# Kernel tuning notes

Hardware: AMD Instinct MI355X
Metric: run time of the kernel (lower is better)

The kernel has to match this reference:

```python
import jax, jax.numpy as jnp
import numpy as np

D_MODEL, N_HEAD, D_HEAD = 192, 16, 6
INNER = N_HEAD * D_HEAD  # 96
LN_EPS = 1e-9
INF = 1e6


def _rel_pos_embeds(S):
    # Funnel get_position_embeds, relative_shift path, block 0
    half = D_MODEL // 2
    freq = jnp.arange(half, dtype=jnp.float32)
    inv_freq = 1.0 / (10000.0 ** (freq / half))
    rel_pos_id = jnp.arange(-2 * S, 2 * S, dtype=jnp.float32)  # [4S]
    sinusoid = rel_pos_id[:, None] * inv_freq[None, :]          # [4S, half]
    pos_embed = jnp.concatenate([jnp.sin(sinusoid), jnp.cos(sinusoid)], axis=-1)  # [4S, D]
    # block 0: relative_pos(pos, stride=1) = arange(S, -S, -1), offset by 2S
    idx = jnp.arange(S, -S, -1) + 2 * S  # [2S]
    return pos_embed[idx]  # [2S, D]


def _relative_shift_gather(pos_attn, context_len):
    # shift = 1 (q_len == context_len)
    B, n, S, M = pos_attn.shape  # M = 2*S
    pa = pos_attn.reshape(B, n, M, S)[:, :, 1:, :]
    pa = pa.reshape(B, n, S, M - 1)[..., :context_len]
    return pa


def setup_inputs() -> dict:
    key = jax.random.key(0)
    ks = jax.random.split(key, 12)
    B, S = 4, 1024
    s = 0.02
    return {
        "x": jax.random.normal(ks[0], (B, S, D_MODEL), dtype=jnp.float32),
        "mask0": jnp.ones((B, S), dtype=jnp.float32),
        "Wq": jax.random.normal(ks[1], (D_MODEL, INNER), dtype=jnp.float32) * s,
        "Wk": jax.random.normal(ks[2], (D_MODEL, INNER), dtype=jnp.float32) * s,
        "bk": jnp.zeros((INNER,), dtype=jnp.float32),
        "Wv": jax.random.normal(ks[3], (D_MODEL, INNER), dtype=jnp.float32) * s,
        "bv": jnp.zeros((INNER,), dtype=jnp.float32),
        "Wo": jax.random.normal(ks[4], (INNER, D_MODEL), dtype=jnp.float32) * s,
        "bo": jnp.zeros((D_MODEL,), dtype=jnp.float32),
        "r_w_bias": jax.random.normal(ks[5], (N_HEAD, D_HEAD), dtype=jnp.float32) * s,
        "r_r_bias": jax.random.normal(ks[6], (N_HEAD, D_HEAD), dtype=jnp.float32) * s,
        "r_kernel": jax.random.normal(ks[7], (D_MODEL, N_HEAD, D_HEAD), dtype=jnp.float32) * s,
        "gamma": jnp.ones((D_MODEL,), dtype=jnp.float32),
        "beta": jnp.zeros((D_MODEL,), dtype=jnp.float32),
    }


def reference(x, mask0, Wq, Wk, bk, Wv, bv, Wo, bo, r_w_bias, r_r_bias, r_kernel, gamma, beta):
    B, S, _ = x.shape
    scale = 1.0 / np.sqrt(D_HEAD).astype(np.float32)

    q = (x @ Wq).reshape(B, S, N_HEAD, D_HEAD) * scale       # q_head pre-scaled
    k = (x @ Wk + bk).reshape(B, S, N_HEAD, D_HEAD)
    v = (x @ Wv + bv).reshape(B, S, N_HEAD, D_HEAD)

    # content score
    content = jnp.einsum("bind,bjnd->bnij", q + r_w_bias * scale, k)

    # positional score with relative shift
    r = _rel_pos_embeds(S)                                    # [2S, D]
    r_head = jnp.einsum("td,dnh->tnh", r, r_kernel)           # [2S, n, h]
    pos_attn = jnp.einsum("binh,tnh->bnit", q + r_r_bias * scale, r_head)  # [B,n,S,2S]
    pos_attn = _relative_shift_gather(pos_attn, S)            # [B,n,S,S]

    attn_score = content + pos_attn  # token_type_attn = 0 (no token_type_ids)
    attn_score = attn_score - INF * (1.0 - mask0[:, None, None, :])
    attn_prob = jax.nn.softmax(attn_score, axis=-1)

    attn_vec = jnp.einsum("bnij,bjnd->bind", attn_prob, v)    # [B,S,n,h]
    attn_out = attn_vec.reshape(B, S, INNER) @ Wo + bo

    h = x + attn_out
    mu = jnp.mean(h, axis=-1, keepdims=True)
    var = jnp.mean(jnp.square(h - mu), axis=-1, keepdims=True)
    out = (h - mu) / jnp.sqrt(var + LN_EPS) * gamma + beta
    return out
```

## Files before the change

kernel.cpp:

```cpp
#include <hip/hip_runtime.h>
#include <hip/hip_bf16.h>
#include <math.h>

#define LOG2E 1.4426950408889634f
#define IS6   0.4082482904638630f

typedef _Float16 h2 __attribute__((ext_vector_type(2)));

#if defined(__has_builtin)
#if __has_builtin(__builtin_amdgcn_fdot2)
#define FDOT2(a,b,c) __builtin_amdgcn_fdot2((a),(b),(c),false)
#endif
#endif
#ifndef FDOT2
#define FDOT2(a,b,c) ((float)(a).x*(float)(b).x + (float)(a).y*(float)(b).y + (c))
#endif

__device__ __forceinline__ unsigned packh2(float x, float y) {
    h2 v; v.x = (_Float16)x; v.y = (_Float16)y;
    return *(unsigned*)&v;
}
__device__ __forceinline__ h2 ash2(unsigned u) { return *(h2*)&u; }
__device__ __forceinline__ unsigned ah2(h2 v) { return *(unsigned*)&v; }

__device__ __forceinline__ float fdot2_asm(h2 a, h2 b, float c) {
    float d;
    asm("v_dot2_f32_f16 %0, %1, %2, %3" : "=v"(d) : "v"(a), "v"(b), "v"(c));
    return d;
}
__device__ __forceinline__ float exp2_asm(float x) {
    float r;
    asm("v_exp_f32 %0, %1" : "=v"(r) : "v"(x));
    return r;
}

#if defined(__has_builtin)
#if __has_builtin(__builtin_amdgcn_cvt_pkrtz)
__device__ __forceinline__ h2 pk2(float a, float b) {
    auto r = __builtin_amdgcn_cvt_pkrtz(a, b);
    union { decltype(r) f; h2 h; } c; c.f = r; return c.h;
}
#define HAVE_PK2 1
#endif
#endif
#ifndef HAVE_PK2
__device__ __forceinline__ h2 pk2(float a, float b) {
    h2 v; v.x = (_Float16)a; v.y = (_Float16)b; return v;
}
#endif

__global__ __launch_bounds__(256)
void k_pre(const float* __restrict__ x,
           const float* __restrict__ Wq, const float* __restrict__ Wk,
           const float* __restrict__ Wv,
           const float* __restrict__ bk, const float* __restrict__ bv,
           const float* __restrict__ rwb, const float* __restrict__ rrb,
           const float* __restrict__ rk,
           unsigned* __restrict__ QWt, unsigned* __restrict__ QRt,
           unsigned* __restrict__ Kpl, unsigned* __restrict__ Vpl,
           unsigned short* __restrict__ phiB) {
    __shared__ unsigned xs[64 * 97];
    __shared__ uint4 Wlds[384];
    __shared__ float rrowS[4 * 192];
    int tid = threadIdx.x;
    if (blockIdx.x < 512) {
        int t0 = blockIdx.x * 4;
        for (int idx = tid; idx < 768; idx += 256) {
            int tl = idx / 192, d = idx - tl * 192;
            int dd = d < 96 ? d : d - 96;
            float w = exp2f(-(float)dd * 0.13841367062030676f);
            float ang = (float)(1024 - (t0 + tl)) * w;
            rrowS[idx] = (d < 96) ? __sinf(ang) : __cosf(ang);
        }
        __syncthreads();
        if (tid < 192) {
            int c = tid % 96, tg = tid / 96;
            float acc0 = 0.f, acc1 = 0.f;
            #pragma unroll 4
            for (int d = 0; d < 192; ++d) {
                float wv = rk[d * 96 + c];
                acc0 += rrowS[(tg * 2 + 0) * 192 + d] * wv;
                acc1 += rrowS[(tg * 2 + 1) * 192 + d] * wv;
            }
            int n = c / 6, h = c - n * 6;
            _Float16 v0 = (_Float16)acc0, v1 = (_Float16)acc1;
            phiB[(n * 2048 + t0 + tg * 2 + 0) * 8 + h] = *(unsigned short*)&v0;
            phiB[(n * 2048 + t0 + tg * 2 + 1) * 8 + h] = *(unsigned short*)&v1;
            if (tg == 0 && c < 32) {
                int nn = c >> 1, hh = 6 + (c & 1);
                #pragma unroll
                for (int k = 0; k < 4; ++k)
                    phiB[(nn * 2048 + t0 + k) * 8 + hh] = 0;
            }
        }
    } else {
        int qkvb = blockIdx.x - 512;
        int rt = qkvb / 18, qb = qkvb - rt * 18;
        int row0 = rt * 64;
        for (int idx = tid; idx < 6144; idx += 256) {
            int r = idx / 96, dpp = idx - r * 96;
            float2 xv = *(const float2*)&x[(size_t)(row0 + r) * 192 + dpp * 2];
            xs[r * 97 + dpp] = packh2(xv.x, xv.y);
        }
        for (int idx = tid; idx < 384; idx += 256) {
            int quad = idx / 96, dp = idx - quad * 96;
            int cq = qb * 4 + quad;
            int mat = cq / 24, c0 = (cq - mat * 24) * 4;
            const float* W = mat == 0 ? Wq : (mat == 1 ? Wk : Wv);
            float4 r0 = *(const float4*)&W[(2 * dp) * 96 + c0];
            float4 r1 = *(const float4*)&W[(2 * dp + 1) * 96 + c0];
            uint4 v;
            v.x = packh2(r0.x, r1.x);
            v.y = packh2(r0.y, r1.y);
            v.z = packh2(r0.z, r1.z);
            v.w = packh2(r0.w, r1.w);
            Wlds[idx] = v;
        }
        __syncthreads();
        int quad = __builtin_amdgcn_readfirstlane(tid >> 6);
        int sl = tid & 63;
        int cq = qb * 4 + quad;
        int c0g = cq * 4;
        int mat = c0g / 96, col0 = c0g - mat * 96;
        const uint4* wb = &Wlds[quad * 96];
        const unsigned* xr = xs + sl * 97;
        float a0 = 0.f, a1 = 0.f, a2 = 0.f, a3 = 0.f;
        #pragma unroll 8
        for (int dp = 0; dp < 96; ++dp) {
            uint4 w4 = wb[dp];
            h2 xp = ash2(xr[dp]);
            a0 = FDOT2(xp, ash2(w4.x), a0);
            a1 = FDOT2(xp, ash2(w4.y), a1);
            a2 = FDOT2(xp, ash2(w4.z), a2);
            a3 = FDOT2(xp, ash2(w4.w), a3);
        }
        float av[4] = {a0, a1, a2, a3};
        int row = row0 + sl, b = row >> 10, s = row & 1023;
        if (mat == 0) {
            #pragma unroll
            for (int pp = 0; pp < 2; ++pp) {
                int cA = col0 + 2 * pp;
                int pg = cA >> 1;
                int nn = pg / 3, hp = pg - nn * 3;
                int bnn = b * 16 + nn;
                unsigned qw = packh2((av[2*pp]   + rwb[cA])   * (IS6 * LOG2E),
                                     (av[2*pp+1] + rwb[cA+1]) * (IS6 * LOG2E));
                unsigned qr = packh2((av[2*pp]   + rrb[cA])   * (IS6 * LOG2E),
                                     (av[2*pp+1] + rrb[cA+1]) * (IS6 * LOG2E));
                size_t qo = ((size_t)(hp * 64 + bnn) << 10) + s;
                QWt[qo] = qw;
                QRt[qo] = qr;
            }
        } else if (mat == 1) {
            #pragma unroll
            for (int pp = 0; pp < 2; ++pp) {
                int cA = col0 + 2 * pp;
                int pg = cA >> 1;
                int nn = pg / 3, hp = pg - nn * 3;
                int bnn = b * 16 + nn;
                Kpl[((size_t)(hp * 64 + bnn) << 10) + s] =
                    packh2(av[2*pp] + bk[cA], av[2*pp+1] + bk[cA+1]);
            }
        } else {
            #pragma unroll
            for (int pp = 0; pp < 2; ++pp) {
                int cA = col0 + 2 * pp;
                int pg = cA >> 1;
                int nn = pg / 3, hp = pg - nn * 3;
                int bnn = b * 16 + nn;
                Vpl[((size_t)(hp * 64 + bnn) << 10) + s] =
                    packh2(av[2*pp] + bv[cA], av[2*pp+1] + bv[cA+1]);
            }
        }
    }
}

#define SWZ(r) ((r) ^ (((r) >> 2) & 7))
__global__ __launch_bounds__(256, 4)
void k_attn(const unsigned* __restrict__ QWt, const unsigned* __restrict__ QRt,
            const unsigned* __restrict__ Kpl, const unsigned* __restrict__ Vpl,
            const float* __restrict__ mask0,
            const unsigned short* __restrict__ phiB,
            uint4* __restrict__ P) {
    __shared__ uint4 phiS[1088];
    __shared__ uint4 kS[65];
    __shared__ uint4 vS[65];
    int tid = threadIdx.x;
    int jc = blockIdx.x, n = blockIdx.y, b = blockIdx.z;
    int j0 = jc * 64;
    int bn = b * 16 + n;

    const uint4* phg = (const uint4*)phiB + (n * 2048 + j0 + 1);
    for (int r = tid; r < 1088; r += 256) phiS[SWZ(r)] = phg[r];
    if (tid < 64) {
        int j = j0 + tid;
        size_t base = ((size_t)bn << 10) + j;
        float mt = 1e6f * (mask0[b * 1024 + j] - 1.0f) * LOG2E;
        kS[tid] = make_uint4(Kpl[base], Kpl[base + 65536], Kpl[base + 131072],
                             __float_as_uint(mt));
    } else if (tid < 128) {
        int r = tid - 64;
        int j = j0 + r;
        size_t base = ((size_t)bn << 10) + j;
        vS[r] = make_uint4(Vpl[base], Vpl[base + 65536], Vpl[base + 131072], 0u);
    } else if (tid == 128) {
        kS[64] = make_uint4(0u, 0u, 0u, 0u);
        vS[64] = make_uint4(0u, 0u, 0u, 0u);
    }
    __syncthreads();

    int iA = tid * 4;
    h2 qw[4][3], qr[4][3];
    #pragma unroll
    for (int hp = 0; hp < 3; ++hp) {
        size_t off = (size_t)hp * 65536 + ((size_t)bn << 10) + iA;
        uint4 qa = *(const uint4*)&QWt[off];
        qw[0][hp] = ash2(qa.x); qw[1][hp] = ash2(qa.y);
        qw[2][hp] = ash2(qa.z); qw[3][hp] = ash2(qa.w);
        uint4 ra = *(const uint4*)&QRt[off];
        qr[0][hp] = ash2(ra.x); qr[1][hp] = ash2(ra.y);
        qr[2][hp] = ash2(ra.z); qr[3][hp] = ash2(ra.w);
    }

    float den[4] = {0.f, 0.f, 0.f, 0.f};
    h2 zero2; zero2.x = (_Float16)0.f; zero2.y = (_Float16)0.f;
    h2 ac0[4], ac1[4], ac2[4];
    #pragma unroll
    for (int q = 0; q < 4; ++q) { ac0[q] = zero2; ac1[q] = zero2; ac2[q] = zero2; }

    int Cb = 1023 - iA;
    uint4 ph[4];
    ph[3] = phiS[SWZ(Cb - 1)];
    ph[2] = phiS[SWZ(Cb - 2)];
    ph[1] = phiS[SWZ(Cb - 3)];
    uint4 nxt = phiS[SWZ(Cb)];
    uint4 Kc = kS[0], Vc = vS[0];

    #pragma unroll 4
    for (int jj = 0; jj < 64; ++jj) {
        uint4 K = Kc, V = Vc;
        ph[jj & 3] = nxt;
        Kc = kS[jj + 1];
        Vc = vS[jj + 1];
        nxt = phiS[SWZ(Cb + jj + 1)];
        float mt = __uint_as_float(K.w);
        h2 v01 = ash2(V.x), v23 = ash2(V.y), v45 = ash2(V.z);
        #pragma unroll
        for (int q = 0; q < 4; ++q) {
            uint4 p = ph[(jj - q) & 3];
            float sc = fdot2_asm(ash2(K.x), qw[q][0],
                       fdot2_asm(ash2(K.y), qw[q][1],
                       fdot2_asm(ash2(K.z), qw[q][2], mt)));
            sc = fdot2_asm(ash2(p.x), qr[q][0],
                 fdot2_asm(ash2(p.y), qr[q][1],
                 fdot2_asm(ash2(p.z), qr[q][2], sc)));
            float e = exp2_asm(sc);
            den[q] += e;
            h2 e2 = pk2(e, e);
            ac0[q] += e2 * v01;
            ac1[q] += e2 * v23;
            ac2[q] += e2 * v45;
        }
    }
    size_t pb = ((size_t)(jc * 64 + bn)) << 10;
    #pragma unroll
    for (int q = 0; q < 4; ++q) {
        uint4 st;
        st.x = __float_as_uint(den[q]);
        st.y = ah2(ac0[q]); st.z = ah2(ac1[q]); st.w = ah2(ac2[q]);
        P[pb + q * 256 + tid] = st;
    }
}

__global__ __launch_bounds__(256)
void k_out(const uint4* __restrict__ P, const float* __restrict__ Wo,
           const float* __restrict__ bo, const float* __restrict__ x,
           const float* __restrict__ gamma, const float* __restrict__ beta,
           float* __restrict__ out) {
    __shared__ unsigned WoS[96 * 96];
    __shared__ float avS[8 * 96];
    int tid = threadIdx.x;
    int row0 = blockIdx.x * 8;
    for (int idx = tid; idx < 9216; idx += 256) {
        int c = idx / 96, pd = idx - c * 96;
        float2 w = *(const float2*)&Wo[c * 192 + pd * 2];
        WoS[idx] = packh2(w.x, w.y);
    }
    if (tid < 128) {
        int n = tid >> 3, rl = tid & 7;
        int row = row0 + rl, b = row >> 10, i = row & 1023;
        int bn = b * 16 + n;
        int q = i & 3, tt = i >> 2;
        float d = 0.f, s0 = 0.f, s1 = 0.f, s2 = 0.f, s3 = 0.f, s4 = 0.f, s5 = 0.f;
        #pragma unroll
        for (int jc = 0; jc < 16; ++jc) {
            uint4 u = P[(((size_t)(jc * 64 + bn)) << 10) + q * 256 + tt];
            h2 x0 = ash2(u.y), x1 = ash2(u.z), x2 = ash2(u.w);
            d  += __uint_as_float(u.x);
            s0 += (float)x0.x; s1 += (float)x0.y;
            s2 += (float)x1.x; s3 += (float)x1.y;
            s4 += (float)x2.x; s5 += (float)x2.y;
        }
        float inv = 1.0f / d;
        float* o = &avS[rl * 96 + n * 6];
        o[0] = s0 * inv; o[1] = s1 * inv; o[2] = s2 * inv;
        o[3] = s3 * inv; o[4] = s4 * inv; o[5] = s5 * inv;
    }
    __syncthreads();

    int lane = tid & 63, wv = tid >> 6;
    bool act = lane < 48;
    int d0 = lane * 4;
    #pragma unroll
    for (int rr = 0; rr < 2; ++rr) {
        int r = wv * 2 + rr, row = row0 + r;
        float ax = 0.f, ay = 0.f, az = 0.f, aw = 0.f;
        if (act) {
            float4 bq = *(const float4*)&bo[d0];
            float4 xq = *(const float4*)&x[(size_t)row * 192 + d0];
            ax = bq.x + xq.x; ay = bq.y + xq.y; az = bq.z + xq.z; aw = bq.w + xq.w;
            for (int c2 = 0; c2 < 96; ++c2) {
                float a = avS[r * 96 + c2];
                uint2 wp = *(uint2*)&WoS[c2 * 96 + lane * 2];
                h2 w0 = ash2(wp.x), w1 = ash2(wp.y);
                ax += a * (float)w0.x; ay += a * (float)w0.y;
                az += a * (float)w1.x; aw += a * (float)w1.y;
            }
        }
        float sum = act ? (ax + ay + az + aw) : 0.f;
        #pragma unroll
        for (int off = 32; off; off >>= 1) sum += __shfl_xor(sum, off, 64);
        float mu = sum * (1.0f / 192.0f);
        float dx = ax - mu, dy = ay - mu, dz = az - mu, dw = aw - mu;
        float vs = act ? (dx * dx + dy * dy + dz * dz + dw * dw) : 0.f;
        #pragma unroll
        for (int off = 32; off; off >>= 1) vs += __shfl_xor(vs, off, 64);
        float rstd = rsqrtf(vs * (1.0f / 192.0f) + 1e-9f);
        if (act) {
            float4 g = *(const float4*)&gamma[d0];
            float4 bb = *(const float4*)&beta[d0];
            float4 rv;
            rv.x = dx * rstd * g.x + bb.x;
            rv.y = dy * rstd * g.y + bb.y;
            rv.z = dz * rstd * g.z + bb.z;
            rv.w = dw * rstd * g.w + bb.w;
            *(float4*)&out[(size_t)row * 192 + d0] = rv;
        }
    }
}

extern "C" void kernel_launch(void* const* d_in, const int* in_sizes, int n_in,
                              void* d_out, int out_size, void* d_ws, size_t ws_size,
                              hipStream_t stream) {
    const float* x        = (const float*)d_in[0];
    const float* mask0    = (const float*)d_in[1];
    const float* Wq       = (const float*)d_in[2];
    const float* Wk       = (const float*)d_in[3];
    const float* bk       = (const float*)d_in[4];
    const float* Wv       = (const float*)d_in[5];
    const float* bv       = (const float*)d_in[6];
    const float* Wo       = (const float*)d_in[7];
    const float* bo       = (const float*)d_in[8];
    const float* rwb      = (const float*)d_in[9];
    const float* rrb      = (const float*)d_in[10];
    const float* r_kernel = (const float*)d_in[11];
    const float* gamma    = (const float*)d_in[12];
    const float* beta     = (const float*)d_in[13];
    float* out = (float*)d_out;

    unsigned* QWt = (unsigned*)d_ws;
    unsigned* QRt = QWt + 196608;
    unsigned* Kpl = QRt + 196608;
    unsigned* Vpl = Kpl + 196608;
    uint4*    P   = (uint4*)(Vpl + 196608);
    unsigned short* phiB = (unsigned short*)(P + 1048576);

    k_pre<<<1664, 256, 0, stream>>>(x, Wq, Wk, Wv, bk, bv, rwb, rrb, r_kernel,
                                    QWt, QRt, Kpl, Vpl, phiB);
    k_attn<<<dim3(16, 16, 4), 256, 0, stream>>>(QWt, QRt, Kpl, Vpl, mask0, phiB, P);
    k_out<<<512, 256, 0, stream>>>(P, Wo, bo, x, gamma, beta, out);
}
```

Baseline: 94.69 us.

## Split partial-sum combine into separate kernel and unroll attention loop with static ring slots

The attention inner loop is manually unrolled by four with compile-time ring-buffer slot indices, so the phi registers need no dynamic indexing. The cross-chunk combine of partial softmax sums moves out of k_out into a new k_comb kernel, where all threads do coalesced reads of P and write normalized attention vectors to a workspace buffer. k_out then just loads those rows. This aims to drop the half-idle, strided combine inside k_out, at the cost of an extra kernel launch and an extra global round trip for AV.

```diff
diff --git a/kernel.cpp b/kernel.cpp
--- a/kernel.cpp
+++ b/kernel.cpp
@@ -236,32 +236,45 @@
     uint4 nxt = phiS[SWZ(Cb)];
     uint4 Kc = kS[0], Vc = vS[0];
 
-    #pragma unroll 4
-    for (int jj = 0; jj < 64; ++jj) {
-        uint4 K = Kc, V = Vc;
-        ph[jj & 3] = nxt;
-        Kc = kS[jj + 1];
-        Vc = vS[jj + 1];
-        nxt = phiS[SWZ(Cb + jj + 1)];
-        float mt = __uint_as_float(K.w);
-        h2 v01 = ash2(V.x), v23 = ash2(V.y), v45 = ash2(V.z);
-        #pragma unroll
-        for (int q = 0; q < 4; ++q) {
-            uint4 p = ph[(jj - q) & 3];
-            float sc = fdot2_asm(ash2(K.x), qw[q][0],
-                       fdot2_asm(ash2(K.y), qw[q][1],
-                       fdot2_asm(ash2(K.z), qw[q][2], mt)));
-            sc = fdot2_asm(ash2(p.x), qr[q][0],
-                 fdot2_asm(ash2(p.y), qr[q][1],
-                 fdot2_asm(ash2(p.z), qr[q][2], sc)));
-            float e = exp2_asm(sc);
-            den[q] += e;
-            h2 e2 = pk2(e, e);
-            ac0[q] += e2 * v01;
-            ac1[q] += e2 * v23;
-            ac2[q] += e2 * v45;
-        }
-    }
+#define SCORE_AT(slot, qq)                                                      \
+    {                                                                           \
+        uint4 p = ph[slot];                                                     \
+        float sc = fdot2_asm(ash2(K.x), qw[qq][0],                              \
+                   fdot2_asm(ash2(K.y), qw[qq][1],                              \
+                   fdot2_asm(ash2(K.z), qw[qq][2], mt)));                       \
+        sc = fdot2_asm(ash2(p.x), qr[qq][0],                                    \
+             fdot2_asm(ash2(p.y), qr[qq][1],                                    \
+             fdot2_asm(ash2(p.z), qr[qq][2], sc)));                             \
+        float e = exp2_asm(sc);                                                 \
+        den[qq] += e;                                                           \
+        h2 e2 = pk2(e, e);                                                      \
+        ac0[qq] += e2 * v01;                                                    \
+        ac1[qq] += e2 * v23;                                                    \
+        ac2[qq] += e2 * v45;                                                    \
+    }
+
+#define STEP(kk, s0_, s1_, s2_, s3_)                                            \
+    {                                                                           \
+        const int jj = j4 + (kk);                                               \
+        uint4 K = Kc, V = Vc;                                                   \
+        ph[kk] = nxt;                                                           \
+        Kc = kS[jj + 1];                                                        \
+        Vc = vS[jj + 1];                                                        \
+        nxt = phiS[SWZ(Cb + jj + 1)];                                           \
+        float mt = __uint_as_float(K.w);                                        \
+        h2 v01 = ash2(V.x), v23 = ash2(V.y), v45 = ash2(V.z);                   \
+        SCORE_AT(s0_, 0) SCORE_AT(s1_, 1) SCORE_AT(s2_, 2) SCORE_AT(s3_, 3)     \
+    }
+
+    for (int j4 = 0; j4 < 64; j4 += 4) {
+        STEP(0, 0, 3, 2, 1)
+        STEP(1, 1, 0, 3, 2)
+        STEP(2, 2, 1, 0, 3)
+        STEP(3, 3, 2, 1, 0)
+    }
+#undef STEP
+#undef SCORE_AT
+
     size_t pb = ((size_t)(jc * 64 + bn)) << 10;
     #pragma unroll
     for (int q = 0; q < 4; ++q) {
@@ -273,7 +286,30 @@
 }
 
 __global__ __launch_bounds__(256)
-void k_out(const uint4* __restrict__ P, const float* __restrict__ Wo,
+void k_comb(const uint4* __restrict__ P, float* __restrict__ AV) {
+    int flat = blockIdx.x * 256 + threadIdx.x;
+    int bn = flat >> 10, rem = flat & 1023;
+    int q = rem >> 8, tt = rem & 255;
+    int i = tt * 4 + q;
+    int b = bn >> 4, n = bn & 15;
+    float d = 0.f, s0 = 0.f, s1 = 0.f, s2 = 0.f, s3 = 0.f, s4 = 0.f, s5 = 0.f;
+    #pragma unroll
+    for (int jc = 0; jc < 16; ++jc) {
+        uint4 u = P[(((size_t)(jc * 64 + bn)) << 10) + rem];
+        h2 x0 = ash2(u.y), x1 = ash2(u.z), x2 = ash2(u.w);
+        d  += __uint_as_float(u.x);
+        s0 += (float)x0.x; s1 += (float)x0.y;
+        s2 += (float)x1.x; s3 += (float)x1.y;
+        s4 += (float)x2.x; s5 += (float)x2.y;
+    }
+    float inv = 1.0f / d;
+    float* o = AV + ((size_t)(b * 1024 + i)) * 96 + n * 6;
+    o[0] = s0 * inv; o[1] = s1 * inv; o[2] = s2 * inv;
+    o[3] = s3 * inv; o[4] = s4 * inv; o[5] = s5 * inv;
+}
+
+__global__ __launch_bounds__(256)
+void k_out(const float* __restrict__ AV, const float* __restrict__ Wo,
            const float* __restrict__ bo, const float* __restrict__ x,
            const float* __restrict__ gamma, const float* __restrict__ beta,
            float* __restrict__ out) {
@@ -286,26 +322,8 @@
         float2 w = *(const float2*)&Wo[c * 192 + pd * 2];
         WoS[idx] = packh2(w.x, w.y);
     }
-    if (tid < 128) {
-        int n = tid >> 3, rl = tid & 7;
-        int row = row0 + rl, b = row >> 10, i = row & 1023;
-        int bn = b * 16 + n;
-        int q = i & 3, tt = i >> 2;
-        float d = 0.f, s0 = 0.f, s1 = 0.f, s2 = 0.f, s3 = 0.f, s4 = 0.f, s5 = 0.f;
-        #pragma unroll
-        for (int jc = 0; jc < 16; ++jc) {
-            uint4 u = P[(((size_t)(jc * 64 + bn)) << 10) + q * 256 + tt];
-            h2 x0 = ash2(u.y), x1 = ash2(u.z), x2 = ash2(u.w);
-            d  += __uint_as_float(u.x);
-            s0 += (float)x0.x; s1 += (float)x0.y;
-            s2 += (float)x1.x; s3 += (float)x1.y;
-            s4 += (float)x2.x; s5 += (float)x2.y;
-        }
-        float inv = 1.0f / d;
-        float* o = &avS[rl * 96 + n * 6];
-        o[0] = s0 * inv; o[1] = s1 * inv; o[2] = s2 * inv;
-        o[3] = s3 * inv; o[4] = s4 * inv; o[5] = s5 * inv;
-    }
+    for (int idx = tid; idx < 768; idx += 256)
+        avS[idx] = AV[(size_t)row0 * 96 + idx];
     __syncthreads();
 
     int lane = tid & 63, wv = tid >> 6;
@@ -374,9 +392,11 @@
     unsigned* Vpl = Kpl + 196608;
     uint4*    P   = (uint4*)(Vpl + 196608);
     unsigned short* phiB = (unsigned short*)(P + 1048576);
+    float*    AV  = (float*)(phiB + 262144);
 
     k_pre<<<1664, 256, 0, stream>>>(x, Wq, Wk, Wv, bk, bv, rwb, rrb, r_kernel,
                                     QWt, QRt, Kpl, Vpl, phiB);
     k_attn<<<dim3(16, 16, 4), 256, 0, stream>>>(QWt, QRt, Kpl, Vpl, mask0, phiB, P);
-    k_out<<<512, 256, 0, stream>>>(P, Wo, bo, x, gamma, beta, out);
-}
+    k_comb<<<256, 256, 0, stream>>>(P, AV);
+    k_out<<<512, 256, 0, stream>>>(AV, Wo, bo, x, gamma, beta, out);
+}
```

Measured after the change: 89.50 us (median of 2 runs). -5.5%, faster.
